# Kernel optimization log

Measured on AMD Instinct MI355X. Metric: run time of the kernel, lower is better.

Reference implementation:

```python
import jax, jax.numpy as jnp
import numpy as np

PPU = 64          # points_per_unit
MARGIN = 0.1
INIT_LENGTHSCALE = 0.1


def setup_inputs() -> dict:
    key = jax.random.key(0)
    k1, k2, k3 = jax.random.split(key, 3)
    m, nc, nt, dim, dy = 8, 1024, 512, 2, 2
    xc = jax.random.uniform(k1, (m, nc, dim), jnp.float32)
    yc = jax.random.normal(k2, (m, nc, dy), jnp.float32)
    xt = jax.random.uniform(k3, (m, nt, dim), jnp.float32)
    # lengthscale_param = log(exp(init_ls) - 1) so softplus(param) == init_ls
    lengthscale_param = jnp.log(jnp.expm1(jnp.full((dim,), INIT_LENGTHSCALE, jnp.float32)))
    return {"xc": xc, "yc": yc, "xt": xt, "lengthscale_param": lengthscale_param}


def reference(xc, yc, xt, lengthscale_param):
    m, _, dim = xc.shape
    lengthscale = 1e-5 + jax.nn.softplus(lengthscale_param)  # (dim,)

    # append density channel of ones
    yc1 = jnp.concatenate([yc, jnp.ones(yc.shape[:-1] + (1,), yc.dtype)], axis=-1)

    # adaptive grid over concat(xc, xt)
    x_all = jnp.concatenate([xc, xt], axis=-2)
    xmin = x_all.min(axis=-2)  # (m, dim)
    xmax = x_all.max(axis=-2)  # (m, dim)
    Nf = jnp.ceil((0.5 * (xmax - xmin) + MARGIN) * PPU).max(axis=0)
    Nf = 2.0 ** jnp.ceil(jnp.log2(Nf))
    N = np.asarray(Nf).astype(np.int64)  # concrete per-dim half-widths (grid size)

    axes = [jnp.arange(-int(n), int(n) + 1, dtype=xc.dtype) for n in N]  # inclusive, like torch.range
    base = jnp.stack(jnp.meshgrid(*axes, indexing='ij'), axis=-1)  # (n1,...,ndim, dim)
    x_mid = 0.5 * (xmin + xmax)  # (m, dim)
    x_grid = x_mid.reshape((m,) + (1,) * dim + (dim,)) + base[None] / PPU  # (m, n1,...,ndim, dim)
    x_grid_flat = x_grid.reshape(m, -1, dim)  # (m, ng, dim)

    # RBF weights: exp(-0.5 * ||(g - c)/ls||^2) via expanded quadratic form
    a = x_grid_flat / lengthscale  # (m, ng, dim)
    b = xc / lengthscale           # (m, nc, dim)
    dist2 = ((a * a).sum(-1)[:, :, None]
             + (b * b).sum(-1)[:, None, :]
             - 2.0 * jnp.einsum('bgd,bcd->bgc', a, b))
    weights = jnp.exp(-0.5 * jnp.maximum(dist2, 0.0))  # (m, ng, nc)

    z_flat = weights @ yc1  # (m, ng, dy+1)
    z_grid = z_flat.reshape(x_grid.shape[:-1] + (yc1.shape[-1],))
    return (x_grid, z_grid)
```

## Files before the change

### kernel.cpp

```cpp
#include <hip/hip_runtime.h>
#include <math.h>

#define M_BATCH 8
#define NC 1024
#define NTGT 512
#define G_DIM 129
#define NG (G_DIM * G_DIM)
#define N_OUT (G_DIM * 3)
#define TM 32
#define TN 32
#define KCH 128
#define NKCH (NC / KCH)
#define LDA 136
#define MT_TILES 5
#define NT_TILES 13
#define ABYTES (TM * LDA * 2)

typedef __attribute__((ext_vector_type(8))) _Float16 half8;
typedef __attribute__((ext_vector_type(2))) _Float16 half2v;
typedef __attribute__((ext_vector_type(4))) float floatx4;

#if defined(__has_builtin)
#if __has_builtin(__builtin_amdgcn_exp2f)
#define FAST_EXP2(x) __builtin_amdgcn_exp2f(x)
#endif
#endif
#ifndef FAST_EXP2
#define FAST_EXP2(x) exp2f(x)
#endif

__global__ __launch_bounds__(512) void fused_kernel(
        const float* __restrict__ xc, const float* __restrict__ yc,
        const float* __restrict__ xt, const float* __restrict__ lsp,
        float* __restrict__ out_grid, float* __restrict__ out_z) {
    const int tid = threadIdx.x;
    const int t = blockIdx.x;
    const int m = blockIdx.y;
    const int mt = t / NT_TILES;
    const int nt = t - mt * NT_TILES;

    __shared__ __align__(16) char lds_raw[4 * ABYTES];

    {
        float mn0 = 1e30f, mx0 = -1e30f, mn1 = 1e30f, mx1 = -1e30f;
        const float2* pc = (const float2*)(xc + m * NC * 2);
        for (int i = tid; i < NC; i += 512) {
            float2 p = pc[i];
            mn0 = fminf(mn0, p.x); mx0 = fmaxf(mx0, p.x);
            mn1 = fminf(mn1, p.y); mx1 = fmaxf(mx1, p.y);
        }
        const float2* pt = (const float2*)(xt + m * NTGT * 2);
        {
            float2 p = pt[tid];
            mn0 = fminf(mn0, p.x); mx0 = fmaxf(mx0, p.x);
            mn1 = fminf(mn1, p.y); mx1 = fmaxf(mx1, p.y);
        }
        float4* sm = (float4*)lds_raw;
        sm[tid] = make_float4(mn0, mx0, mn1, mx1);
    }
    __syncthreads();
    {
        float4* sm = (float4*)lds_raw;
        for (int s = 256; s > 0; s >>= 1) {
            if (tid < s) {
                float4 a = sm[tid], b = sm[tid + s];
                sm[tid] = make_float4(fminf(a.x, b.x), fmaxf(a.y, b.y),
                                      fminf(a.z, b.z), fmaxf(a.w, b.w));
            }
            __syncthreads();
        }
    }
    const float mid0 = 0.5f * (((float4*)lds_raw)[0].x + ((float4*)lds_raw)[0].y);
    const float mid1 = 0.5f * (((float4*)lds_raw)[0].z + ((float4*)lds_raw)[0].w);
    __syncthreads();

    const float Kc = 0.84932180028801904272f;
    const float ls0 = 1e-5f + log1pf(expf(lsp[0]));
    const float ls1 = 1e-5f + log1pf(expf(lsp[1]));
    const float s0 = Kc / ls0, s1 = Kc / ls1;
    const float inv_ppu = 1.0f / 64.0f;

    if (nt == 0) {
        const int r0 = mt * TM;
        const int nrows = min(TM, G_DIM - r0);
        float2* og = (float2*)out_grid + (size_t)m * NG;
        for (int g = tid; g < nrows * G_DIM; g += 512) {
            const int r = g / G_DIM;
            const int iyy = g - r * G_DIM;
            const int ixg = r0 + r;
            og[(size_t)ixg * G_DIM + iyy] =
                make_float2(mid0 + (float)(ixg - 64) * inv_ppu,
                            mid1 + (float)(iyy - 64) * inv_ppu);
        }
    }

    const int c2 = (tid & 63) * 2;
    const int r0s = tid >> 6;
    const float4* xc4 = (const float4*)(xc + m * NC * 2);
    const float4* yc4 = (const float4*)(yc + m * NC * 2);
    const float gxs_base = (mid0 + (float)(mt * TM - 64) * inv_ppu) * s0;
    const float gstep = inv_ppu * s0;

    const int w = tid >> 6;
    const int g = w >> 2;
    const int wm = (w >> 1) & 1;
    const int wn = w & 1;
    const int lane = tid & 63;
    const int ln = lane & 15;
    const int q = lane >> 4;

    floatx4 acc = {0.f, 0.f, 0.f, 0.f};

    auto stage = [&](int kc, int buf) {
        const int cp = (kc * KCH >> 1) + (tid & 63);
        const float4 xq = xc4[cp];
        const float4 yq = yc4[cp];
        const float cx0 = xq.x * s0, cx1 = xq.z * s0;
        const float cy0 = xq.y * s1, cy1 = xq.w * s1;
        _Float16* Ab = (_Float16*)(lds_raw + (size_t)buf * 2 * ABYTES);
        _Float16* Bb = (_Float16*)(lds_raw + (size_t)buf * 2 * ABYTES + ABYTES);
#pragma unroll
        for (int i = 0; i < 4; ++i) {
            const int r = r0s + 8 * i;
            const float gxs = gxs_base + (float)r * gstep;
            const float dx0 = gxs - cx0;
            const float dx1 = gxs - cx1;
            *(half2v*)&Ab[r * LDA + c2] =
                (half2v){(_Float16)FAST_EXP2(-(dx0 * dx0)),
                         (_Float16)FAST_EXP2(-(dx1 * dx1))};
            const int n = nt * TN + r;
            const int iy = (int)(((unsigned)n * 0xAAABu) >> 17);
            const int ch = n - 3 * iy;
            const float gys = (mid1 + (float)(iy - 64) * inv_ppu) * s1;
            const float dy0 = gys - cy0;
            const float dy1 = gys - cy1;
            const float wy0 = FAST_EXP2(-(dy0 * dy0));
            const float wy1 = FAST_EXP2(-(dy1 * dy1));
            const float ya = (ch == 0) ? yq.x : (ch == 1) ? yq.y : 1.0f;
            const float yb = (ch == 0) ? yq.z : (ch == 1) ? yq.w : 1.0f;
            *(half2v*)&Bb[r * LDA + c2] =
                (half2v){(_Float16)(wy0 * ya), (_Float16)(wy1 * yb)};
        }
    };

    stage(0, 0);
    __syncthreads();

    for (int kc = 0; kc < NKCH; ++kc) {
        const int buf = kc & 1;
        const _Float16* Ab = (const _Float16*)(lds_raw + (size_t)buf * 2 * ABYTES);
        const _Float16* Bb = (const _Float16*)(lds_raw + (size_t)buf * 2 * ABYTES + ABYTES);
#pragma unroll
        for (int kk = 0; kk < 2; ++kk) {
            half8 a = *(const half8*)&Ab[(wm * 16 + ln) * LDA + g * 64 + kk * 32 + q * 8];
            half8 b = *(const half8*)&Bb[(wn * 16 + ln) * LDA + g * 64 + kk * 32 + q * 8];
            acc = __builtin_amdgcn_mfma_f32_16x16x32_f16(a, b, acc, 0, 0, 0);
        }
        if (kc + 1 < NKCH) stage(kc + 1, buf ^ 1);
        __syncthreads();
    }

    floatx4* cs = (floatx4*)lds_raw;
    if (g == 1) cs[(size_t)(w & 3) * 64 + lane] = acc;
    __syncthreads();
    if (g == 0) {
        const floatx4 o = cs[(size_t)w * 64 + lane];
        const int ngo = nt * TN + wn * 16 + ln;
        if (ngo < N_OUT) {
            float* oz = out_z + (size_t)m * NG * 3;
            const int ixb = mt * TM + wm * 16 + q * 4;
#pragma unroll
            for (int rr = 0; rr < 4; ++rr) {
                const int ixg = ixb + rr;
                if (ixg < G_DIM)
                    oz[(size_t)ixg * N_OUT + ngo] = acc[rr] + o[rr];
            }
        }
    }
}

extern "C" void kernel_launch(void* const* d_in, const int* in_sizes, int n_in,
                              void* d_out, int out_size, void* d_ws, size_t ws_size,
                              hipStream_t stream) {
    const float* xc  = (const float*)d_in[0];
    const float* yc  = (const float*)d_in[1];
    const float* xt  = (const float*)d_in[2];
    const float* lsp = (const float*)d_in[3];

    float* out_grid = (float*)d_out;
    float* out_z = out_grid + (size_t)M_BATCH * NG * 2;

    dim3 grid(MT_TILES * NT_TILES, M_BATCH);
    fused_kernel<<<grid, 512, 0, stream>>>(xc, yc, xt, lsp, out_grid, out_z);
}
```

Baseline: 73.24 us.

## Share y-weight tile across three channels and multiply by y inside MFMA loop

Measured after the change: 67.82 us. -7.4%, faster.

```diff
diff --git a/kernel.cpp b/kernel.cpp
--- a/kernel.cpp
+++ b/kernel.cpp
@@ -8,13 +8,13 @@
 #define NG (G_DIM * G_DIM)
 #define N_OUT (G_DIM * 3)
 #define TM 32
-#define TN 32
+#define TIY 32
 #define KCH 128
 #define NKCH (NC / KCH)
 #define LDA 136
-#define MT_TILES 5
-#define NT_TILES 13
 #define ABYTES (TM * LDA * 2)
+#define BUFBYTES (2 * ABYTES + 512)
+#define GT 5
 
 typedef __attribute__((ext_vector_type(8))) _Float16 half8;
 typedef __attribute__((ext_vector_type(2))) _Float16 half2v;
@@ -34,12 +34,11 @@
         const float* __restrict__ xt, const float* __restrict__ lsp,
         float* __restrict__ out_grid, float* __restrict__ out_z) {
     const int tid = threadIdx.x;
-    const int t = blockIdx.x;
-    const int m = blockIdx.y;
-    const int mt = t / NT_TILES;
-    const int nt = t - mt * NT_TILES;
-
-    __shared__ __align__(16) char lds_raw[4 * ABYTES];
+    const int iyt = blockIdx.x;
+    const int mt = blockIdx.y;
+    const int m  = blockIdx.z;
+
+    __shared__ __align__(16) char lds_raw[2 * BUFBYTES];
 
     {
         float mn0 = 1e30f, mx0 = -1e30f, mn1 = 1e30f, mx1 = -1e30f;
@@ -55,8 +54,7 @@
             mn0 = fminf(mn0, p.x); mx0 = fmaxf(mx0, p.x);
             mn1 = fminf(mn1, p.y); mx1 = fmaxf(mx1, p.y);
         }
-        float4* sm = (float4*)lds_raw;
-        sm[tid] = make_float4(mn0, mx0, mn1, mx1);
+        ((float4*)lds_raw)[tid] = make_float4(mn0, mx0, mn1, mx1);
     }
     __syncthreads();
     {
@@ -80,7 +78,7 @@
     const float s0 = Kc / ls0, s1 = Kc / ls1;
     const float inv_ppu = 1.0f / 64.0f;
 
-    if (nt == 0) {
+    if (iyt == 0) {
         const int r0 = mt * TM;
         const int nrows = min(TM, G_DIM - r0);
         float2* og = (float2*)out_grid + (size_t)m * NG;
@@ -99,7 +97,9 @@
     const float4* xc4 = (const float4*)(xc + m * NC * 2);
     const float4* yc4 = (const float4*)(yc + m * NC * 2);
     const float gxs_base = (mid0 + (float)(mt * TM - 64) * inv_ppu) * s0;
-    const float gstep = inv_ppu * s0;
+    const float gys_base = (mid1 + (float)(iyt * TIY - 64) * inv_ppu) * s1;
+    const float gstep_x = inv_ppu * s0;
+    const float gstep_y = inv_ppu * s1;
 
     const int w = tid >> 6;
     const int g = w >> 2;
@@ -109,37 +109,39 @@
     const int ln = lane & 15;
     const int q = lane >> 4;
 
-    floatx4 acc = {0.f, 0.f, 0.f, 0.f};
+    floatx4 acc0 = {0.f, 0.f, 0.f, 0.f};
+    floatx4 acc1 = {0.f, 0.f, 0.f, 0.f};
+    floatx4 acc2 = {0.f, 0.f, 0.f, 0.f};
 
     auto stage = [&](int kc, int buf) {
-        const int cp = (kc * KCH >> 1) + (tid & 63);
+        const int cp = kc * 64 + (tid & 63);
         const float4 xq = xc4[cp];
         const float4 yq = yc4[cp];
         const float cx0 = xq.x * s0, cx1 = xq.z * s0;
         const float cy0 = xq.y * s1, cy1 = xq.w * s1;
-        _Float16* Ab = (_Float16*)(lds_raw + (size_t)buf * 2 * ABYTES);
-        _Float16* Bb = (_Float16*)(lds_raw + (size_t)buf * 2 * ABYTES + ABYTES);
+        _Float16* Ab  = (_Float16*)(lds_raw + buf * BUFBYTES);
+        _Float16* Wyb = (_Float16*)(lds_raw + buf * BUFBYTES + ABYTES);
+        _Float16* yeb = (_Float16*)(lds_raw + buf * BUFBYTES + 2 * ABYTES);
+        _Float16* yob = yeb + 128;
 #pragma unroll
         for (int i = 0; i < 4; ++i) {
             const int r = r0s + 8 * i;
-            const float gxs = gxs_base + (float)r * gstep;
+            const float gxs = gxs_base + (float)r * gstep_x;
             const float dx0 = gxs - cx0;
             const float dx1 = gxs - cx1;
             *(half2v*)&Ab[r * LDA + c2] =
                 (half2v){(_Float16)FAST_EXP2(-(dx0 * dx0)),
                          (_Float16)FAST_EXP2(-(dx1 * dx1))};
-            const int n = nt * TN + r;
-            const int iy = (int)(((unsigned)n * 0xAAABu) >> 17);
-            const int ch = n - 3 * iy;
-            const float gys = (mid1 + (float)(iy - 64) * inv_ppu) * s1;
+            const float gys = gys_base + (float)r * gstep_y;
             const float dy0 = gys - cy0;
             const float dy1 = gys - cy1;
-            const float wy0 = FAST_EXP2(-(dy0 * dy0));
-            const float wy1 = FAST_EXP2(-(dy1 * dy1));
-            const float ya = (ch == 0) ? yq.x : (ch == 1) ? yq.y : 1.0f;
-            const float yb = (ch == 0) ? yq.z : (ch == 1) ? yq.w : 1.0f;
-            *(half2v*)&Bb[r * LDA + c2] =
-                (half2v){(_Float16)(wy0 * ya), (_Float16)(wy1 * yb)};
+            *(half2v*)&Wyb[r * LDA + c2] =
+                (half2v){(_Float16)FAST_EXP2(-(dy0 * dy0)),
+                         (_Float16)FAST_EXP2(-(dy1 * dy1))};
+        }
+        if (tid < 64) {
+            *(half2v*)&yeb[c2] = (half2v){(_Float16)yq.x, (_Float16)yq.z};
+            *(half2v*)&yob[c2] = (half2v){(_Float16)yq.y, (_Float16)yq.w};
         }
     };
 
@@ -148,32 +150,49 @@
 
     for (int kc = 0; kc < NKCH; ++kc) {
         const int buf = kc & 1;
-        const _Float16* Ab = (const _Float16*)(lds_raw + (size_t)buf * 2 * ABYTES);
-        const _Float16* Bb = (const _Float16*)(lds_raw + (size_t)buf * 2 * ABYTES + ABYTES);
+        const _Float16* Ab  = (const _Float16*)(lds_raw + buf * BUFBYTES);
+        const _Float16* Wyb = (const _Float16*)(lds_raw + buf * BUFBYTES + ABYTES);
+        const _Float16* yeb = (const _Float16*)(lds_raw + buf * BUFBYTES + 2 * ABYTES);
 #pragma unroll
         for (int kk = 0; kk < 2; ++kk) {
-            half8 a = *(const half8*)&Ab[(wm * 16 + ln) * LDA + g * 64 + kk * 32 + q * 8];
-            half8 b = *(const half8*)&Bb[(wn * 16 + ln) * LDA + g * 64 + kk * 32 + q * 8];
-            acc = __builtin_amdgcn_mfma_f32_16x16x32_f16(a, b, acc, 0, 0, 0);
+            const int off = g * 64 + kk * 32 + q * 8;
+            half8 a  = *(const half8*)&Ab[(wm * 16 + ln) * LDA + off];
+            half8 wy = *(const half8*)&Wyb[(wn * 16 + ln) * LDA + off];
+            half8 ye = *(const half8*)&yeb[off];
+            half8 yo = *(const half8*)&yeb[128 + off];
+            acc2 = __builtin_amdgcn_mfma_f32_16x16x32_f16(a, wy, acc2, 0, 0, 0);
+            acc0 = __builtin_amdgcn_mfma_f32_16x16x32_f16(a, wy * ye, acc0, 0, 0, 0);
+            acc1 = __builtin_amdgcn_mfma_f32_16x16x32_f16(a, wy * yo, acc1, 0, 0, 0);
         }
         if (kc + 1 < NKCH) stage(kc + 1, buf ^ 1);
         __syncthreads();
     }
 
     floatx4* cs = (floatx4*)lds_raw;
-    if (g == 1) cs[(size_t)(w & 3) * 64 + lane] = acc;
+    const int ws = wm * 2 + wn;
+    if (g == 1) {
+        cs[(ws * 3 + 0) * 64 + lane] = acc0;
+        cs[(ws * 3 + 1) * 64 + lane] = acc1;
+        cs[(ws * 3 + 2) * 64 + lane] = acc2;
+    }
     __syncthreads();
     if (g == 0) {
-        const floatx4 o = cs[(size_t)w * 64 + lane];
-        const int ngo = nt * TN + wn * 16 + ln;
-        if (ngo < N_OUT) {
-            float* oz = out_z + (size_t)m * NG * 3;
+        const floatx4 o0 = cs[(ws * 3 + 0) * 64 + lane];
+        const floatx4 o1 = cs[(ws * 3 + 1) * 64 + lane];
+        const floatx4 o2 = cs[(ws * 3 + 2) * 64 + lane];
+        const int iyg = iyt * TIY + wn * 16 + ln;
+        if (iyg < G_DIM) {
+            float* oz = out_z + (size_t)m * NG * 3 + (size_t)iyg * 3;
             const int ixb = mt * TM + wm * 16 + q * 4;
 #pragma unroll
             for (int rr = 0; rr < 4; ++rr) {
                 const int ixg = ixb + rr;
-                if (ixg < G_DIM)
-                    oz[(size_t)ixg * N_OUT + ngo] = acc[rr] + o[rr];
+                if (ixg < G_DIM) {
+                    float* p = oz + (size_t)ixg * N_OUT;
+                    p[0] = acc0[rr] + o0[rr];
+                    p[1] = acc1[rr] + o1[rr];
+                    p[2] = acc2[rr] + o2[rr];
+                }
             }
         }
     }
@@ -190,6 +209,6 @@
     float* out_grid = (float*)d_out;
     float* out_z = out_grid + (size_t)M_BATCH * NG * 2;
 
-    dim3 grid(MT_TILES * NT_TILES, M_BATCH);
+    dim3 grid(GT, GT, M_BATCH);
     fused_kernel<<<grid, 512, 0, stream>>>(xc, yc, xt, lsp, out_grid, out_z);
 }
```
